# Kernel tuning notes

Hardware: AMD Instinct MI355X
Metric: run time of the kernel (lower is better)

## Reference

```python
import jax, jax.numpy as jnp
import numpy as np

B, T, I, S, H = 32, 8192, 256, 256, 256
NEG = 1e30


def setup_inputs() -> dict:
    key = jax.random.key(0)
    ks = jax.random.split(key, 8)
    x = jax.random.normal(ks[0], (B, T, I), dtype=jnp.float32)
    init = jax.random.normal(ks[1], (B, S), dtype=jnp.float32)
    mask = (jax.random.uniform(ks[2], (B, T)) > 0.1).astype(jnp.float32)
    W1 = jax.random.normal(ks[3], (H, S + I), dtype=jnp.float32) * (1.0 / np.sqrt(S + I))
    W2 = jax.random.normal(ks[4], (1, H), dtype=jnp.float32) * (1.0 / np.sqrt(H))
    w_ih = jax.random.normal(ks[5], (3 * S, I), dtype=jnp.float32) * (1.0 / np.sqrt(I))
    w_hh = jax.random.normal(ks[6], (3 * S, S), dtype=jnp.float32) * (1.0 / np.sqrt(S))
    b_ih = jnp.zeros((3 * S,), dtype=jnp.float32)
    b_hh = jnp.zeros((3 * S,), dtype=jnp.float32)
    return {"x": x, "init": init, "mask": mask, "W1": W1, "W2": W2,
            "w_ih": w_ih, "w_hh": w_hh, "b_ih": b_ih, "b_hh": b_hh}


def _pointer(x, state, mask, W1, W2):
    # concat([state_expanded, input], dim=2) @ W1.T == state @ W1[:, :S].T + x @ W1[:, S:].T
    Ws, Wi = W1[:, :S], W1[:, S:]
    h = jnp.tanh(jnp.einsum('bti,hi->bth', x, Wi) + (state @ Ws.T)[:, None, :])  # [B,T,H]
    att = jnp.einsum('bth,oh->bto', h, W2)[..., 0]  # [B,T]
    logit = att - NEG * (1.0 - mask)
    p = jax.nn.softmax(logit, axis=1)
    out = jnp.einsum('bt,bti->bi', p, x)
    return out, logit


def _gru_cell(inp, h, w_ih, w_hh, b_ih, b_hh):
    gi = inp @ w_ih.T + b_ih  # [B, 3S]
    gh = h @ w_hh.T + b_hh
    i_r, i_z, i_n = jnp.split(gi, 3, axis=1)
    h_r, h_z, h_n = jnp.split(gh, 3, axis=1)
    r = jax.nn.sigmoid(i_r + h_r)
    z = jax.nn.sigmoid(i_z + h_z)
    n = jnp.tanh(i_n + r * h_n)
    return (1.0 - z) * n + z * h


def reference(x, init, mask, W1, W2, w_ih, w_hh, b_ih, b_hh):
    # eval mode: all dropout masks are identity (dropout=0.0)
    out, logit1 = _pointer(x, init, mask, W1, W2)
    state = _gru_cell(out, init, w_ih, w_hh, b_ih, b_hh)
    _, logit2 = _pointer(x, state, mask, W1, W2)
    return (logit1, logit2)
```

## Files before the change

kernel.cpp:

```cpp
#include <hip/hip_runtime.h>
#include <hip/hip_bf16.h>
#include <stdint.h>

#define BB 32
#define TT 8192
#define II 256
#define SS 256
#define HH 256
#define NEGC 1e30f

typedef __bf16 bf16x8 __attribute__((ext_vector_type(8)));
typedef __bf16 bf16x4 __attribute__((ext_vector_type(4)));
typedef float f32x4 __attribute__((ext_vector_type(4)));

__device__ __forceinline__ float fast_tanh(float x) {
    float e = __expf(2.f * x);
    return 1.f - 2.f * __builtin_amdgcn_rcpf(e + 1.f);
}
__device__ __forceinline__ float fast_sigmoid(float x) {
    return __builtin_amdgcn_rcpf(1.f + __expf(-x));
}

__global__ __launch_bounds__(256) void wi_cvt_kernel(const float* __restrict__ W1,
                                                     __bf16* __restrict__ wi) {
    int idx = blockIdx.x * 256 + threadIdx.x;
    int h = idx >> 8, k = idx & 255;
    wi[idx] = (__bf16)W1[h * 512 + 256 + k];
}

__global__ __launch_bounds__(256) void sws_slice_kernel(const float* __restrict__ state,
                                                        const float* __restrict__ W1,
                                                        float* __restrict__ sws) {
    __shared__ float sv[32 * 257];
    int tid = threadIdx.x;
    for (int e = tid; e < 8192; e += 256) {
        int b = e >> 8, s = e & 255;
        sv[b * 257 + s] = state[b * 256 + s];
    }
    __syncthreads();
    int hl = tid >> 4, bg = tid & 15;
    int h = blockIdx.x * 16 + hl;
    const float* w1r = W1 + (size_t)h * 512;
    float a0 = 0.f, a1 = 0.f;
#pragma unroll 4
    for (int s = 0; s < 256; ++s) {
        float w = w1r[s];
        a0 += w * sv[(bg * 2 + 0) * 257 + s];
        a1 += w * sv[(bg * 2 + 1) * 257 + s];
    }
    sws[(bg * 2 + 0) * 256 + h] = a0;
    sws[(bg * 2 + 1) * 256 + h] = a1;
}

template <int MODE>
__global__ __launch_bounds__(256, 3) void att_kernel(
    const float* __restrict__ x, const __bf16* __restrict__ xbf_in,
    __bf16* __restrict__ xbf_out, const __bf16* __restrict__ wi,
    const float* __restrict__ w2, const float* __restrict__ sws,
    const float* __restrict__ mask, float* __restrict__ logit_out) {
    __shared__ char xs[64 * 512];
    __shared__ float attp[4][64];

    const int tid = threadIdx.x;
    const int lane = tid & 63, w = tid >> 6;
    const size_t rowbase = (size_t)blockIdx.x * 64;
    const int b = (int)(rowbase >> 13);

    if (MODE == 1) {
        const char* src = (const char*)xbf_in + rowbase * 512;
#pragma unroll
        for (int it = 0; it < 8; ++it) {
            int L = (it * 256 + tid) * 16;
            bf16x8 v = *(const bf16x8*)(src + L);
            int row = L >> 9, kb = L & 511;
            *(bf16x8*)(xs + row * 512 + (kb ^ ((row & 7) << 4))) = v;
        }
    } else {
        const float* src = x + rowbase * 256;
#pragma unroll
        for (int it = 0; it < 8; ++it) {
            int L = (it * 256 + tid) * 16;
            int e = L >> 1;
            float4 f0 = *(const float4*)(src + e);
            float4 f1 = *(const float4*)(src + e + 4);
            bf16x8 v;
            v[0] = (__bf16)f0.x; v[1] = (__bf16)f0.y; v[2] = (__bf16)f0.z; v[3] = (__bf16)f0.w;
            v[4] = (__bf16)f1.x; v[5] = (__bf16)f1.y; v[6] = (__bf16)f1.z; v[7] = (__bf16)f1.w;
            int row = L >> 9, kb = L & 511;
            *(bf16x8*)(xs + row * 512 + (kb ^ ((row & 7) << 4))) = v;
            if (MODE == 0)
                *(bf16x8*)((char*)xbf_out + rowbase * 512 + L) = v;
        }
    }
    __syncthreads();

    const int l15 = lane & 15, lg = lane >> 4;
    f32x4 acc[4][4] = {};
    const char* wib = (const char*)wi + (size_t)(w * 64 + l15) * 512 + lg * 16;
#pragma unroll
    for (int kk = 0; kk < 8; ++kk) {
        bf16x8 bfrag[4];
#pragma unroll
        for (int fn = 0; fn < 4; ++fn)
            bfrag[fn] = *(const bf16x8*)(wib + fn * 16 * 512 + kk * 64);
        bf16x8 afrag[4];
#pragma unroll
        for (int fm = 0; fm < 4; ++fm) {
            int row = fm * 16 + l15;
            int kb = kk * 64 + lg * 16;
            afrag[fm] = *(const bf16x8*)(xs + row * 512 + (kb ^ ((row & 7) << 4)));
        }
#pragma unroll
        for (int fm = 0; fm < 4; ++fm)
#pragma unroll
            for (int fn = 0; fn < 4; ++fn)
                acc[fm][fn] = __builtin_amdgcn_mfma_f32_16x16x32_bf16(
                    afrag[fm], bfrag[fn], acc[fm][fn], 0, 0, 0);
    }

    float w2v[4], swsv[4];
#pragma unroll
    for (int fn = 0; fn < 4; ++fn) {
        int h = w * 64 + fn * 16 + l15;
        w2v[fn] = w2[h];
        swsv[fn] = sws[b * 256 + h];
    }
    const bool hi8 = (l15 & 8) != 0, hi4 = (l15 & 4) != 0;
    const int ridx = ((l15 & 8) >> 2) | ((l15 & 4) >> 2);
#pragma unroll
    for (int fm = 0; fm < 4; ++fm) {
        float part[4];
#pragma unroll
        for (int r = 0; r < 4; ++r) {
            float s = 0.f;
#pragma unroll
            for (int fn = 0; fn < 4; ++fn) {
                float hv = acc[fm][fn][r] + swsv[fn];
                s += w2v[fn] * fast_tanh(hv);
            }
            part[r] = s;
        }
        float s0 = hi8 ? part[0] : part[2];
        float s1 = hi8 ? part[1] : part[3];
        float r0 = __shfl_xor(s0, 8, 64);
        float r1 = __shfl_xor(s1, 8, 64);
        float a0 = (hi8 ? part[2] : part[0]) + r0;
        float a1 = (hi8 ? part[3] : part[1]) + r1;
        float s2 = hi4 ? a0 : a1;
        float r2 = __shfl_xor(s2, 4, 64);
        float bsum = (hi4 ? a1 : a0) + r2;
        bsum += __shfl_xor(bsum, 2, 64);
        bsum += __shfl_xor(bsum, 1, 64);
        if ((l15 & 3) == 0) attp[w][fm * 16 + lg * 4 + ridx] = bsum;
    }
    __syncthreads();
    if (tid < 64) {
        float att = attp[0][tid] + attp[1][tid] + attp[2][tid] + attp[3][tid];
        float mv = mask[rowbase + tid];
        logit_out[rowbase + tid] = att - NEGC * (1.f - mv);
    }
}

__global__ __launch_bounds__(256) void chunkstat_kernel(const float* __restrict__ logit,
                                                        float2* __restrict__ stat) {
    __shared__ float redm[4], reds[4];
    int bc = blockIdx.x, tid = threadIdx.x;
    const float* lp = logit + (size_t)bc * 1024;
    float4 v = *(const float4*)(lp + tid * 4);
    float m = fmaxf(fmaxf(v.x, v.y), fmaxf(v.z, v.w));
#pragma unroll
    for (int o = 1; o < 64; o <<= 1) m = fmaxf(m, __shfl_xor(m, o, 64));
    if ((tid & 63) == 0) redm[tid >> 6] = m;
    __syncthreads();
    m = fmaxf(fmaxf(redm[0], redm[1]), fmaxf(redm[2], redm[3]));
    float s = __expf(v.x - m) + __expf(v.y - m) + __expf(v.z - m) + __expf(v.w - m);
#pragma unroll
    for (int o = 1; o < 64; o <<= 1) s += __shfl_xor(s, o, 64);
    if ((tid & 63) == 0) reds[tid >> 6] = s;
    __syncthreads();
    if (tid == 0) {
        float2 st;
        st.x = m;
        st.y = reds[0] + reds[1] + reds[2] + reds[3];
        stat[bc] = st;
    }
}

template <int MODE>
__global__ __launch_bounds__(256) void outpart_kernel(
    const float* __restrict__ logit, const float2* __restrict__ stat,
    const float* __restrict__ xf, const __bf16* __restrict__ xbf,
    float* __restrict__ out_part) {
    int b = blockIdx.x >> 3, c = blockIdx.x & 7;
    int tid = threadIdx.x;
    int ig = tid & 63, tg = tid >> 6;
    __shared__ float pl[1024];
    __shared__ float sacc[4][256];
    float m = -3.4e38f;
#pragma unroll
    for (int cc = 0; cc < 8; ++cc) m = fmaxf(m, stat[b * 8 + cc].x);
    float ssum = 0.f;
#pragma unroll
    for (int cc = 0; cc < 8; ++cc) {
        float2 st = stat[b * 8 + cc];
        ssum += st.y * __expf(st.x - m);
    }
    float invs = 1.f / ssum;
    const size_t tbase = (size_t)b * TT + (size_t)c * 1024;
    for (int t = tid; t < 1024; t += 256)
        pl[t] = __expf(logit[tbase + t] - m) * invs;
    __syncthreads();
    float a0 = 0, a1 = 0, a2 = 0, a3 = 0;
    if (MODE == 0) {
        const __bf16* xp = xbf + tbase * 256 + ig * 4;
        for (int t = tg; t < 1024; t += 4) {
            float pv = pl[t];
            bf16x4 v = *(const bf16x4*)(xp + (size_t)t * 256);
            a0 += pv * (float)v[0];
            a1 += pv * (float)v[1];
            a2 += pv * (float)v[2];
            a3 += pv * (float)v[3];
        }
    } else {
        const float* xp = xf + tbase * 256 + ig * 4;
        for (int t = tg; t < 1024; t += 4) {
            float pv = pl[t];
            float4 v = *(const float4*)(xp + (size_t)t * 256);
            a0 += pv * v.x;
            a1 += pv * v.y;
            a2 += pv * v.z;
            a3 += pv * v.w;
        }
    }
    sacc[tg][ig * 4 + 0] = a0;
    sacc[tg][ig * 4 + 1] = a1;
    sacc[tg][ig * 4 + 2] = a2;
    sacc[tg][ig * 4 + 3] = a3;
    __syncthreads();
    if (tid < 256) {
        float s = sacc[0][tid] + sacc[1][tid] + sacc[2][tid] + sacc[3][tid];
        out_part[(size_t)(b * 8 + c) * 256 + tid] = s;
    }
}

__global__ __launch_bounds__(256) void gru_gemm_kernel(
    const float* __restrict__ out_part, const float* __restrict__ init,
    const float* __restrict__ w_ih, const float* __restrict__ w_hh,
    const float* __restrict__ b_ih, const float* __restrict__ b_hh,
    float* __restrict__ gi, float* __restrict__ gh) {
    __shared__ float outv[32 * 257];
    __shared__ float initv[32 * 257];
    int tid = threadIdx.x;
    for (int e = tid; e < 8192; e += 256) {
        int b = e >> 8, i = e & 255;
        float o = 0.f;
#pragma unroll
        for (int c = 0; c < 8; ++c) o += out_part[(size_t)(b * 8 + c) * 256 + i];
        outv[b * 257 + i] = o;
        initv[b * 257 + i] = init[b * 256 + i];
    }
    __syncthreads();
    int kl = tid >> 4, bg = tid & 15;
    int k = blockIdx.x * 16 + kl;
    const float* wir = w_ih + (size_t)k * 256;
    const float* whr = w_hh + (size_t)k * 256;
    float gia0 = b_ih[k], gia1 = gia0;
    float gha0 = b_hh[k], gha1 = gha0;
#pragma unroll 4
    for (int i = 0; i < 256; ++i) {
        float wiv = wir[i], whv = whr[i];
        gia0 += wiv * outv[(bg * 2 + 0) * 257 + i];
        gia1 += wiv * outv[(bg * 2 + 1) * 257 + i];
        gha0 += whv * initv[(bg * 2 + 0) * 257 + i];
        gha1 += whv * initv[(bg * 2 + 1) * 257 + i];
    }
    gi[k * 32 + bg * 2 + 0] = gia0;
    gi[k * 32 + bg * 2 + 1] = gia1;
    gh[k * 32 + bg * 2 + 0] = gha0;
    gh[k * 32 + bg * 2 + 1] = gha1;
}

__global__ __launch_bounds__(256) void gru_point_kernel(
    const float* __restrict__ gi, const float* __restrict__ gh,
    const float* __restrict__ init, float* __restrict__ state) {
    int b = blockIdx.x, s = threadIdx.x;
    float gir = gi[s * 32 + b], giz = gi[(256 + s) * 32 + b], gin = gi[(512 + s) * 32 + b];
    float ghr = gh[s * 32 + b], ghz = gh[(256 + s) * 32 + b], ghn = gh[(512 + s) * 32 + b];
    float r = fast_sigmoid(gir + ghr);
    float z = fast_sigmoid(giz + ghz);
    float n = fast_tanh(gin + r * ghn);
    float h0 = init[b * 256 + s];
    state[b * 256 + s] = (1.f - z) * n + z * h0;
}

extern "C" void kernel_launch(void* const* d_in, const int* in_sizes, int n_in,
                              void* d_out, int out_size, void* d_ws, size_t ws_size,
                              hipStream_t stream) {
    const float* x = (const float*)d_in[0];
    const float* init = (const float*)d_in[1];
    const float* mask = (const float*)d_in[2];
    const float* W1 = (const float*)d_in[3];
    const float* W2 = (const float*)d_in[4];
    const float* w_ih = (const float*)d_in[5];
    const float* w_hh = (const float*)d_in[6];
    const float* b_ih = (const float*)d_in[7];
    const float* b_hh = (const float*)d_in[8];
    float* out = (float*)d_out;

    char* ws = (char*)d_ws;
    size_t off = 0;
    auto alloc = [&](size_t sz) {
        char* p = ws + off;
        off += (sz + 255) & ~(size_t)255;
        return p;
    };
    __bf16* wi = (__bf16*)alloc((size_t)HH * II * 2);
    float* sws1 = (float*)alloc(BB * 256 * 4);
    float* sws2 = (float*)alloc(BB * 256 * 4);
    float* out_part = (float*)alloc(BB * 8 * 256 * 4);
    float2* stat = (float2*)alloc(BB * 8 * 8);
    float* gi_buf = (float*)alloc(768 * 32 * 4);
    float* gh_buf = (float*)alloc(768 * 32 * 4);
    float* state_buf = (float*)alloc(BB * 256 * 4);
    __bf16* xbf = (__bf16*)alloc((size_t)BB * TT * II * 2);
    const bool big = (off <= ws_size);
    (void)in_sizes; (void)n_in; (void)out_size;

    wi_cvt_kernel<<<256, 256, 0, stream>>>(W1, wi);
    sws_slice_kernel<<<16, 256, 0, stream>>>(init, W1, sws1);

    const int ntiles = BB * TT / 64;
    if (big)
        att_kernel<0><<<ntiles, 256, 0, stream>>>(x, nullptr, xbf, wi, W2, sws1, mask, out);
    else
        att_kernel<2><<<ntiles, 256, 0, stream>>>(x, nullptr, nullptr, wi, W2, sws1, mask, out);

    chunkstat_kernel<<<256, 256, 0, stream>>>(out, stat);

    if (big)
        outpart_kernel<0><<<256, 256, 0, stream>>>(out, stat, nullptr, xbf, out_part);
    else
        outpart_kernel<2><<<256, 256, 0, stream>>>(out, stat, x, nullptr, out_part);

    gru_gemm_kernel<<<48, 256, 0, stream>>>(out_part, init, w_ih, w_hh, b_ih, b_hh,
                                            gi_buf, gh_buf);
    gru_point_kernel<<<32, 256, 0, stream>>>(gi_buf, gh_buf, init, state_buf);
    sws_slice_kernel<<<16, 256, 0, stream>>>(state_buf, W1, sws2);

    if (big)
        att_kernel<1><<<ntiles, 256, 0, stream>>>(nullptr, xbf, nullptr, wi, W2, sws2, mask,
                                                  out + (size_t)BB * TT);
    else
        att_kernel<2><<<ntiles, 256, 0, stream>>>(x, nullptr, nullptr, wi, W2, sws2, mask,
                                                  out + (size_t)BB * TT);
}
```

Measured before the change: 649.1 us.

## Split outpart over more blocks, merge prep kernels, prefetch W fragments in att

Merges the bf16 weight conversion and the initial state projection into a single launch. In the attention kernel it hoists the W2/sws loads ahead of the barrier and double-buffers the B-fragment global loads across k-steps. The weighted-sum kernel now splits each batch row into 32 chunks instead of 8, launching 1024 blocks with 8-wide bf16 loads, and a new small reduction kernel sums the partials. This aims to raise parallelism in the memory-bound x pass and to hide load latency, at the cost of one extra launch and more register pressure.

```diff
diff --git a/kernel.cpp b/kernel.cpp
--- a/kernel.cpp
+++ b/kernel.cpp
@@ -21,11 +21,35 @@
     return __builtin_amdgcn_rcpf(1.f + __expf(-x));
 }
 
-__global__ __launch_bounds__(256) void wi_cvt_kernel(const float* __restrict__ W1,
-                                                     __bf16* __restrict__ wi) {
-    int idx = blockIdx.x * 256 + threadIdx.x;
-    int h = idx >> 8, k = idx & 255;
-    wi[idx] = (__bf16)W1[h * 512 + 256 + k];
+__global__ __launch_bounds__(256) void prep_kernel(const float* __restrict__ W1,
+                                                   const float* __restrict__ init,
+                                                   __bf16* __restrict__ wi,
+                                                   float* __restrict__ sws) {
+    __shared__ float sv[32 * 257];
+    int tid = threadIdx.x;
+    if (blockIdx.x < 256) {
+        int idx = blockIdx.x * 256 + tid;
+        int h = idx >> 8, k = idx & 255;
+        wi[idx] = (__bf16)W1[h * 512 + 256 + k];
+        return;
+    }
+    for (int e = tid; e < 8192; e += 256) {
+        int b = e >> 8, s = e & 255;
+        sv[b * 257 + s] = init[b * 256 + s];
+    }
+    __syncthreads();
+    int hl = tid >> 4, bg = tid & 15;
+    int h = (blockIdx.x - 256) * 16 + hl;
+    const float* w1r = W1 + (size_t)h * 512;
+    float a0 = 0.f, a1 = 0.f;
+#pragma unroll 4
+    for (int s = 0; s < 256; ++s) {
+        float w = w1r[s];
+        a0 += w * sv[(bg * 2 + 0) * 257 + s];
+        a1 += w * sv[(bg * 2 + 1) * 257 + s];
+    }
+    sws[(bg * 2 + 0) * 256 + h] = a0;
+    sws[(bg * 2 + 1) * 256 + h] = a1;
 }
 
 __global__ __launch_bounds__(256) void sws_slice_kernel(const float* __restrict__ state,
@@ -92,17 +116,34 @@
                 *(bf16x8*)((char*)xbf_out + rowbase * 512 + L) = v;
         }
     }
-    __syncthreads();
 
     const int l15 = lane & 15, lg = lane >> 4;
+    float w2v[4], swsv[4];
+#pragma unroll
+    for (int fn = 0; fn < 4; ++fn) {
+        int h = w * 64 + fn * 16 + l15;
+        w2v[fn] = w2[h];
+        swsv[fn] = sws[b * 256 + h];
+    }
+
+    __syncthreads();
+
     f32x4 acc[4][4] = {};
     const char* wib = (const char*)wi + (size_t)(w * 64 + l15) * 512 + lg * 16;
+    bf16x8 bnext[4];
+#pragma unroll
+    for (int fn = 0; fn < 4; ++fn)
+        bnext[fn] = *(const bf16x8*)(wib + fn * 8192);
 #pragma unroll
     for (int kk = 0; kk < 8; ++kk) {
-        bf16x8 bfrag[4];
-#pragma unroll
-        for (int fn = 0; fn < 4; ++fn)
-            bfrag[fn] = *(const bf16x8*)(wib + fn * 16 * 512 + kk * 64);
+        bf16x8 bcur[4];
+#pragma unroll
+        for (int fn = 0; fn < 4; ++fn) bcur[fn] = bnext[fn];
+        if (kk < 7) {
+#pragma unroll
+            for (int fn = 0; fn < 4; ++fn)
+                bnext[fn] = *(const bf16x8*)(wib + fn * 8192 + (kk + 1) * 64);
+        }
         bf16x8 afrag[4];
 #pragma unroll
         for (int fm = 0; fm < 4; ++fm) {
@@ -115,16 +156,9 @@
 #pragma unroll
             for (int fn = 0; fn < 4; ++fn)
                 acc[fm][fn] = __builtin_amdgcn_mfma_f32_16x16x32_bf16(
-                    afrag[fm], bfrag[fn], acc[fm][fn], 0, 0, 0);
-    }
-
-    float w2v[4], swsv[4];
-#pragma unroll
-    for (int fn = 0; fn < 4; ++fn) {
-        int h = w * 64 + fn * 16 + l15;
-        w2v[fn] = w2[h];
-        swsv[fn] = sws[b * 256 + h];
-    }
+                    afrag[fm], bcur[fn], acc[fm][fn], 0, 0, 0);
+    }
+
     const bool hi8 = (l15 & 8) != 0, hi4 = (l15 & 4) != 0;
     const int ridx = ((l15 & 8) >> 2) | ((l15 & 4) >> 2);
 #pragma unroll
@@ -191,11 +225,11 @@
     const float* __restrict__ logit, const float2* __restrict__ stat,
     const float* __restrict__ xf, const __bf16* __restrict__ xbf,
     float* __restrict__ out_part) {
-    int b = blockIdx.x >> 3, c = blockIdx.x & 7;
+    int b = blockIdx.x >> 5, c = blockIdx.x & 31;
     int tid = threadIdx.x;
-    int ig = tid & 63, tg = tid >> 6;
-    __shared__ float pl[1024];
-    __shared__ float sacc[4][256];
+    int ig = tid & 31, tg = tid >> 5;
+    __shared__ float pl[256];
+    __shared__ float sacc[8][264];
     float m = -3.4e38f;
 #pragma unroll
     for (int cc = 0; cc < 8; ++cc) m = fmaxf(m, stat[b * 8 + cc].x);
@@ -206,45 +240,48 @@
         ssum += st.y * __expf(st.x - m);
     }
     float invs = 1.f / ssum;
-    const size_t tbase = (size_t)b * TT + (size_t)c * 1024;
-    for (int t = tid; t < 1024; t += 256)
-        pl[t] = __expf(logit[tbase + t] - m) * invs;
-    __syncthreads();
-    float a0 = 0, a1 = 0, a2 = 0, a3 = 0;
+    const size_t tbase = (size_t)b * TT + (size_t)c * 256;
+    pl[tid] = __expf(logit[tbase + tid] - m) * invs;
+    __syncthreads();
+    float a[8] = {};
     if (MODE == 0) {
-        const __bf16* xp = xbf + tbase * 256 + ig * 4;
-        for (int t = tg; t < 1024; t += 4) {
+        const __bf16* xp = xbf + tbase * 256 + ig * 8;
+        for (int t = tg; t < 256; t += 8) {
             float pv = pl[t];
-            bf16x4 v = *(const bf16x4*)(xp + (size_t)t * 256);
-            a0 += pv * (float)v[0];
-            a1 += pv * (float)v[1];
-            a2 += pv * (float)v[2];
-            a3 += pv * (float)v[3];
+            bf16x8 v = *(const bf16x8*)(xp + (size_t)t * 256);
+#pragma unroll
+            for (int j = 0; j < 8; ++j) a[j] += pv * (float)v[j];
         }
     } else {
-        const float* xp = xf + tbase * 256 + ig * 4;
-        for (int t = tg; t < 1024; t += 4) {
+        const float* xp = xf + tbase * 256 + ig * 8;
+        for (int t = tg; t < 256; t += 8) {
             float pv = pl[t];
-            float4 v = *(const float4*)(xp + (size_t)t * 256);
-            a0 += pv * v.x;
-            a1 += pv * v.y;
-            a2 += pv * v.z;
-            a3 += pv * v.w;
-        }
-    }
-    sacc[tg][ig * 4 + 0] = a0;
-    sacc[tg][ig * 4 + 1] = a1;
-    sacc[tg][ig * 4 + 2] = a2;
-    sacc[tg][ig * 4 + 3] = a3;
-    __syncthreads();
-    if (tid < 256) {
-        float s = sacc[0][tid] + sacc[1][tid] + sacc[2][tid] + sacc[3][tid];
-        out_part[(size_t)(b * 8 + c) * 256 + tid] = s;
-    }
+            float4 f0 = *(const float4*)(xp + (size_t)t * 256);
+            float4 f1 = *(const float4*)(xp + (size_t)t * 256 + 4);
+            a[0] += pv * f0.x; a[1] += pv * f0.y; a[2] += pv * f0.z; a[3] += pv * f0.w;
+            a[4] += pv * f1.x; a[5] += pv * f1.y; a[6] += pv * f1.z; a[7] += pv * f1.w;
+        }
+    }
+#pragma unroll
+    for (int j = 0; j < 8; ++j) sacc[tg][ig * 8 + j] = a[j];
+    __syncthreads();
+    float s = 0.f;
+#pragma unroll
+    for (int j = 0; j < 8; ++j) s += sacc[j][tid];
+    out_part[(size_t)(b * 32 + c) * 256 + tid] = s;
+}
+
+__global__ __launch_bounds__(256) void outsum_kernel(const float* __restrict__ out_part,
+                                                     float* __restrict__ out_sum) {
+    int b = blockIdx.x, i = threadIdx.x;
+    float s = 0.f;
+#pragma unroll
+    for (int c = 0; c < 32; ++c) s += out_part[(size_t)(b * 32 + c) * 256 + i];
+    out_sum[b * 256 + i] = s;
 }
 
 __global__ __launch_bounds__(256) void gru_gemm_kernel(
-    const float* __restrict__ out_part, const float* __restrict__ init,
+    const float* __restrict__ out_sum, const float* __restrict__ init,
     const float* __restrict__ w_ih, const float* __restrict__ w_hh,
     const float* __restrict__ b_ih, const float* __restrict__ b_hh,
     float* __restrict__ gi, float* __restrict__ gh) {
@@ -253,10 +290,7 @@
     int tid = threadIdx.x;
     for (int e = tid; e < 8192; e += 256) {
         int b = e >> 8, i = e & 255;
-        float o = 0.f;
-#pragma unroll
-        for (int c = 0; c < 8; ++c) o += out_part[(size_t)(b * 8 + c) * 256 + i];
-        outv[b * 257 + i] = o;
+        outv[b * 257 + i] = out_sum[b * 256 + i];
         initv[b * 257 + i] = init[b * 256 + i];
     }
     __syncthreads();
@@ -317,7 +351,8 @@
     __bf16* wi = (__bf16*)alloc((size_t)HH * II * 2);
     float* sws1 = (float*)alloc(BB * 256 * 4);
     float* sws2 = (float*)alloc(BB * 256 * 4);
-    float* out_part = (float*)alloc(BB * 8 * 256 * 4);
+    float* out_part = (float*)alloc((size_t)BB * 32 * 256 * 4);
+    float* out_sum = (float*)alloc(BB * 256 * 4);
     float2* stat = (float2*)alloc(BB * 8 * 8);
     float* gi_buf = (float*)alloc(768 * 32 * 4);
     float* gh_buf = (float*)alloc(768 * 32 * 4);
@@ -326,8 +361,7 @@
     const bool big = (off <= ws_size);
     (void)in_sizes; (void)n_in; (void)out_size;
 
-    wi_cvt_kernel<<<256, 256, 0, stream>>>(W1, wi);
-    sws_slice_kernel<<<16, 256, 0, stream>>>(init, W1, sws1);
+    prep_kernel<<<272, 256, 0, stream>>>(W1, init, wi, sws1);
 
     const int ntiles = BB * TT / 64;
     if (big)
@@ -338,11 +372,12 @@
     chunkstat_kernel<<<256, 256, 0, stream>>>(out, stat);
 
     if (big)
-        outpart_kernel<0><<<256, 256, 0, stream>>>(out, stat, nullptr, xbf, out_part);
+        outpart_kernel<0><<<1024, 256, 0, stream>>>(out, stat, nullptr, xbf, out_part);
     else
-        outpart_kernel<2><<<256, 256, 0, stream>>>(out, stat, x, nullptr, out_part);
-
-    gru_gemm_kernel<<<48, 256, 0, stream>>>(out_part, init, w_ih, w_hh, b_ih, b_hh,
+        outpart_kernel<2><<<1024, 256, 0, stream>>>(out, stat, x, nullptr, out_part);
+
+    outsum_kernel<<<32, 256, 0, stream>>>(out_part, out_sum);
+    gru_gemm_kernel<<<48, 256, 0, stream>>>(out_sum, init, w_ih, w_hh, b_ih, b_hh,
                                             gi_buf, gh_buf);
     gru_point_kernel<<<32, 256, 0, stream>>>(gi_buf, gh_buf, init, state_buf);
     sws_slice_kernel<<<16, 256, 0, stream>>>(state_buf, W1, sws2);
```

New measurement: 565.0 us. 13.0% less time.
